# Optimization experiments

Measured on AMD Instinct MI355X. Metric: run time of the kernel, lower is better.

Reference implementation:

```python
import jax, jax.numpy as jnp
from jax import lax
import numpy as np

# Dims matching init_kwargs
V = 32000      # vocab
D = 768        # d_model
L = 4          # n_layers
N = 16         # state_size
K = 4          # conv kernel
I = 2 * D      # intermediate = expand * d_model = 1536
DT = (D + 15) // 16  # time_step_rank = 48
BATCH, SEQ = 4, 2048
EPS = 1e-5


def setup_inputs() -> dict:
    key = jax.random.key(0)
    ks = jax.random.split(key, 12)
    s = 0.02
    A_init = jnp.broadcast_to(jnp.arange(1, N + 1, dtype=jnp.float32), (L, I, N))
    return {
        "input_ids": jax.random.randint(ks[0], (BATCH, SEQ), 0, V, dtype=jnp.int32),
        "embed": jax.random.normal(ks[1], (V, D), jnp.float32) * s,        # tied lm_head
        "norm_w": jnp.ones((L, D), jnp.float32),
        "in_proj_w": jax.random.normal(ks[2], (L, 2 * I, D), jnp.float32) * s,
        "conv_w": jax.random.normal(ks[3], (L, I, K), jnp.float32) * s,
        "conv_b": jnp.zeros((L, I), jnp.float32),
        "x_proj_w": jax.random.normal(ks[4], (L, DT + 2 * N, I), jnp.float32) * s,
        "dt_proj_w": jax.random.normal(ks[5], (L, I, DT), jnp.float32) * s,
        "dt_proj_b": jax.random.normal(ks[6], (L, I), jnp.float32) * s,
        "A_log": jnp.log(A_init),
        "D_param": jnp.ones((L, I), jnp.float32),
        "out_proj_w": jax.random.normal(ks[7], (L, D, I), jnp.float32) * s,
        "norm_f_w": jnp.ones((D,), jnp.float32),
    }


def rmsnorm(x, w):
    return x * lax.rsqrt(jnp.mean(x * x, axis=-1, keepdims=True) + EPS) * w


def mamba_mixer(x, in_w, cw, cb, xp_w, dtp_w, dtp_b, a_log, d_par, out_w):
    # x: [B, S, D]
    proj = jnp.einsum('bsd,ed->bse', x, in_w)            # [B, S, 2I]
    u, gate = jnp.split(proj, 2, axis=-1)                # each [B, S, I]
    # causal depthwise conv1d (HF pads K-1 then truncates to S == left pad)
    uc = u.transpose(0, 2, 1)                            # [B, I, S]
    conv = lax.conv_general_dilated(
        uc, cw[:, None, :], window_strides=(1,), padding=[(K - 1, 0)],
        feature_group_count=I, dimension_numbers=('NCH', 'OIH', 'NCH'))
    ut = jax.nn.silu(conv + cb[None, :, None]).transpose(0, 2, 1)  # [B, S, I]
    # SSM parameters
    xdbl = jnp.einsum('bsi,ei->bse', ut, xp_w)           # [B, S, DT+2N]
    dt_r = xdbl[..., :DT]
    Bm = xdbl[..., DT:DT + N]                            # [B, S, N]
    Cm = xdbl[..., DT + N:]                              # [B, S, N]
    dt = jax.nn.softplus(jnp.einsum('bsr,ir->bsi', dt_r, dtp_w) + dtp_b)  # [B, S, I]
    A = -jnp.exp(a_log)                                  # [I, N]

    def step(h, ins):
        dt_t, B_t, C_t, u_t = ins                        # [B,I],[B,N],[B,N],[B,I]
        dA = jnp.exp(dt_t[..., None] * A)                # [B, I, N]
        h = dA * h + (dt_t[..., None] * B_t[:, None, :]) * u_t[..., None]
        y = jnp.einsum('bin,bn->bi', h, C_t)
        return h, y

    h0 = jnp.zeros((x.shape[0], I, N), x.dtype)
    xs = (dt.transpose(1, 0, 2), Bm.transpose(1, 0, 2),
          Cm.transpose(1, 0, 2), ut.transpose(1, 0, 2))
    _, ys = lax.scan(step, h0, xs)                       # [S, B, I]
    y = ys.transpose(1, 0, 2) + ut * d_par               # skip D term
    y = y * jax.nn.silu(gate)
    return jnp.einsum('bsi,di->bsd', y, out_w)           # [B, S, D]


def reference(input_ids, embed, norm_w, in_proj_w, conv_w, conv_b, x_proj_w,
              dt_proj_w, dt_proj_b, A_log, D_param, out_proj_w, norm_f_w):
    h = embed[input_ids]                                 # [B, S, D]
    for l in range(L):
        h = h + mamba_mixer(rmsnorm(h, norm_w[l]), in_proj_w[l], conv_w[l],
                            conv_b[l], x_proj_w[l], dt_proj_w[l], dt_proj_b[l],
                            A_log[l], D_param[l], out_proj_w[l])
    h = rmsnorm(h, norm_f_w)
    # module returns logits[:, -1]; compute only last-token logits (tied lm_head)
    return h[:, -1] @ embed.T                            # [B, V]
```

## Files before the change

### kernel.cpp

```cpp
#include <hip/hip_runtime.h>
#include <hip/hip_bf16.h>

#define Vv 32000
#define Dm 768
#define Lm 4
#define Nst 16
#define Kc 4
#define Im 1536
#define DTr 48
#define Bt 4
#define Sq 2048
#define TOK (Bt*Sq)
#define EPSf 1e-5f
#define NC 64
#define CL 32
#define QROWS (Bt*NC*16)
#define LOG2E 1.4426950408889634f
#define LN2f  0.6931471805599453f

using bf16 = __hip_bfloat16;
typedef __bf16 bf16x8 __attribute__((ext_vector_type(8)));
typedef float f32x4 __attribute__((ext_vector_type(4)));
typedef float f32x2 __attribute__((ext_vector_type(2)));

__device__ __forceinline__ float b2f(bf16 x){ return __bfloat162float(x); }
__device__ __forceinline__ bf16 f2b(float x){ return __float2bfloat16(x); }
__device__ __forceinline__ float us2f(ushort u){ unsigned x = (unsigned)u << 16; return __builtin_bit_cast(float, x); }

__device__ __forceinline__ float ex2(float x){
#if __has_builtin(__builtin_amdgcn_exp2f)
  return __builtin_amdgcn_exp2f(x);
#else
  float r; asm("v_exp_f32 %0, %1" : "=v"(r) : "v"(x)); return r;
#endif
}
__device__ __forceinline__ float vlog2(float x){
#if __has_builtin(__builtin_amdgcn_logf)
  return __builtin_amdgcn_logf(x);
#else
  float r; asm("v_log_f32 %0, %1" : "=v"(r) : "v"(x)); return r;
#endif
}
__device__ __forceinline__ float frcp(float x){
#if __has_builtin(__builtin_amdgcn_rcpf)
  return __builtin_amdgcn_rcpf(x);
#else
  float r; asm("v_rcp_f32 %0, %1" : "=v"(r) : "v"(x)); return r;
#endif
}

#define GLDS(gp, lp) __builtin_amdgcn_global_load_lds( \
    (const __attribute__((address_space(1))) void*)(gp), \
    (__attribute__((address_space(3))) void*)(lp), 16, 0, 0)

__global__ __launch_bounds__(256) void k_cvt(const float* __restrict__ src,
                                             bf16* __restrict__ dst, int n){
  int i = (blockIdx.x*256 + threadIdx.x)*4;
  if (i >= n) return;
  float4 v = *(const float4*)(src + i);
  bf16* o = dst + i;
  o[0]=f2b(v.x); o[1]=f2b(v.y); o[2]=f2b(v.z); o[3]=f2b(v.w);
}

__global__ __launch_bounds__(256) void k_cvt_xpw(const float* __restrict__ src,
                                                 bf16* __restrict__ dst){
  int idx = blockIdx.x*256 + threadIdx.x;
  int l = idx / (128*Im); int rem = idx - l*128*Im;
  int r = rem / Im;       int c = rem - r*Im;
  dst[idx] = (r < 80) ? f2b(src[((size_t)l*80 + r)*Im + c]) : f2b(0.f);
}

__global__ __launch_bounds__(256) void k_cvt_dtw(const float* __restrict__ src,
                                                 bf16* __restrict__ dst){
  int idx = blockIdx.x*256 + threadIdx.x;
  int l = idx / (Im*64); int rem = idx - l*Im*64;
  int r = rem / 64;      int c = rem - r*64;
  dst[idx] = (c < 48) ? f2b(src[((size_t)l*Im + r)*48 + c]) : f2b(0.f);
}

__global__ __launch_bounds__(256) void k_embed(const int* __restrict__ ids,
                                               const float* __restrict__ emb,
                                               float* __restrict__ h){
  int t = blockIdx.x;
  const float4* e = (const float4*)(emb + (size_t)ids[t]*Dm);
  float4* o = (float4*)(h + (size_t)t*Dm);
  if (threadIdx.x < Dm/4) o[threadIdx.x] = e[threadIdx.x];
}

__global__ __launch_bounds__(256) void k_rmsnorm(const float* __restrict__ h,
                                                 const float* __restrict__ w,
                                                 bf16* __restrict__ xb){
  int t = blockIdx.x;
  const float* x = h + (size_t)t*Dm;
  float v[3]; float ss = 0.f;
  #pragma unroll
  for (int j=0;j<3;j++){ v[j] = x[threadIdx.x + j*256]; ss += v[j]*v[j]; }
  #pragma unroll
  for (int off=32; off; off>>=1) ss += __shfl_xor(ss, off);
  __shared__ float sred[4];
  int wave = threadIdx.x>>6, lane = threadIdx.x&63;
  if (lane==0) sred[wave]=ss;
  __syncthreads();
  float tot = sred[0]+sred[1]+sred[2]+sred[3];
  float scale = rsqrtf(tot*(1.f/Dm) + EPSf);
  bf16* o = xb + (size_t)t*Dm;
  #pragma unroll
  for (int j=0;j<3;j++){ int d = threadIdx.x + j*256; o[d] = f2b(v[j]*scale*w[d]); }
}

__global__ __launch_bounds__(256) void k_rms_last(const float* __restrict__ h,
                                                  const float* __restrict__ w,
                                                  float* __restrict__ xf){
  int b = blockIdx.x;
  const float* x = h + ((size_t)b*Sq + (Sq-1))*Dm;
  float v[3]; float ss = 0.f;
  #pragma unroll
  for (int j=0;j<3;j++){ v[j] = x[threadIdx.x + j*256]; ss += v[j]*v[j]; }
  #pragma unroll
  for (int off=32; off; off>>=1) ss += __shfl_xor(ss, off);
  __shared__ float sred[4];
  int wave = threadIdx.x>>6, lane = threadIdx.x&63;
  if (lane==0) sred[wave]=ss;
  __syncthreads();
  float tot = sred[0]+sred[1]+sred[2]+sred[3];
  float scale = rsqrtf(tot*(1.f/Dm) + EPSf);
  float* o = xf + (size_t)b*Dm;
  #pragma unroll
  for (int j=0;j<3;j++){ int d = threadIdx.x + j*256; o[d] = v[j]*scale*w[d]; }
}

template<int MODE>
__global__ __launch_bounds__(256) void k_gemm(const bf16* __restrict__ A,
                                              const bf16* __restrict__ Bw,
                                              void* __restrict__ Cout,
                                              const float* __restrict__ bias,
                                              int M, int N, int K,
                                              int lda, int ldb, int ldc){
  __shared__ __align__(16) ushort Ash[128*32];
  __shared__ __align__(16) ushort Bsh[128*32];
  int tid = threadIdx.x;
  int bm = blockIdx.y, bn = blockIdx.x;
  int wave = tid >> 6, lane = tid & 63;
  int wrow = wave >> 1, wcol = wave & 1;
  int quad = lane >> 4, lq = lane & 15;

  f32x4 acc[4][4];
  #pragma unroll
  for (int a=0;a<4;a++)
    #pragma unroll
    for (int b=0;b<4;b++) acc[a][b] = (f32x4){0.f,0.f,0.f,0.f};

  const ushort* Ag = (const ushort*)A;
  const ushort* Bg = (const ushort*)Bw;

  for (int k0 = 0; k0 < K; k0 += 32) {
    __syncthreads();
    #pragma unroll
    for (int c = tid; c < 512; c += 256) {
      int row = c >> 2, col = (c & 3) * 8;
      GLDS(&Ag[(size_t)(bm*128 + row)*lda + k0 + col], &Ash[c*8]);
      GLDS(&Bg[(size_t)(bn*128 + row)*ldb + k0 + col], &Bsh[c*8]);
    }
    __syncthreads();
    bf16x8 af[4], bfr[4];
    #pragma unroll
    for (int a=0;a<4;a++){
      int m = wrow*64 + a*16 + lq;
      af[a] = __builtin_bit_cast(bf16x8, *(const uint4*)&Ash[m*32 + quad*8]);
    }
    #pragma unroll
    for (int b=0;b<4;b++){
      int n = wcol*64 + b*16 + lq;
      bfr[b] = __builtin_bit_cast(bf16x8, *(const uint4*)&Bsh[n*32 + quad*8]);
    }
    #pragma unroll
    for (int a=0;a<4;a++)
      #pragma unroll
      for (int b=0;b<4;b++)
        acc[a][b] = __builtin_amdgcn_mfma_f32_16x16x32_bf16(af[a], bfr[b], acc[a][b], 0, 0, 0);
  }
  #pragma unroll
  for (int a=0;a<4;a++)
    #pragma unroll
    for (int b=0;b<4;b++)
      #pragma unroll
      for (int r=0;r<4;r++){
        int row = bm*128 + wrow*64 + a*16 + quad*4 + r;
        int col = bn*128 + wcol*64 + b*16 + lq;
        size_t idx = (size_t)row*ldc + col;
        if (MODE == 0) ((bf16*)Cout)[idx] = f2b(acc[a][b][r]);
        else if (MODE == 1) ((float*)Cout)[idx] += acc[a][b][r];
        else {
          float v = acc[a][b][r] + bias[col];
          float sp;
          if (v > 20.f) sp = v;
          else { float e = ex2(v*LOG2E); sp = vlog2(1.f + e)*LN2f; }
          ((bf16*)Cout)[idx] = f2b(sp);
        }
      }
}

#define SA256(qm,k0s,bf_) { GLDS(Ag + sA[qm][0] + (k0s), lds + (bf_)*32768 + lA[qm][0]); \
                            GLDS(Ag + sA[qm][1] + (k0s), lds + (bf_)*32768 + lA[qm][1]); }
#define SB256(qn,k0s,bf_) { GLDS(Bg + sB[qn][0] + (k0s), lds + 65536 + (bf_)*32768 + lB[qn][0]); \
                            GLDS(Bg + sB[qn][1] + (k0s), lds + 65536 + (bf_)*32768 + lB[qn][1]); }
#define RD_A(qm_) do{ _Pragma("unroll") for(int m2=0;m2<4;m2++){ \
    int r = wm*128 + ((qm_)*4+m2)*16 + lq; \
    _Pragma("unroll") for(int kh=0;kh<2;kh++) \
      bA[m2][kh] = *(const uint4*)(Ab + (r<<7) + ((kh*64 + quad*16) ^ ((r&7)<<4))); } }while(0)
#define RD_B(qn_) do{ _Pragma("unroll") for(int n2=0;n2<2;n2++){ \
    int r = wn*64 + ((qn_)*2+n2)*16 + lq; \
    _Pragma("unroll") for(int kh=0;kh<2;kh++) \
      bB[qn_][n2][kh] = *(const uint4*)(Bb + (r<<7) + ((kh*64 + quad*16) ^ ((r&7)<<4))); } }while(0)
#define MMA256(qm_,qn_) do{ \
  __builtin_amdgcn_s_barrier(); \
  __builtin_amdgcn_sched_barrier(0); \
  __builtin_amdgcn_s_setprio(1); \
  _Pragma("unroll") for(int m2=0;m2<4;m2++) \
    _Pragma("unroll") for(int n2=0;n2<2;n2++) \
      _Pragma("unroll") for(int kh=0;kh<2;kh++) \
        acc[(qm_)*4+m2][(qn_)*2+n2] = __builtin_amdgcn_mfma_f32_16x16x32_bf16( \
          __builtin_bit_cast(bf16x8, bA[m2][kh]), __builtin_bit_cast(bf16x8, bB[qn_][n2][kh]), \
          acc[(qm_)*4+m2][(qn_)*2+n2], 0, 0, 0); \
  __builtin_amdgcn_s_setprio(0); \
  __builtin_amdgcn_s_barrier(); \
  __builtin_amdgcn_sched_barrier(0); \
}while(0)
#define VMW4 asm volatile("s_waitcnt vmcnt(4)":::"memory")

template<int MODE>
__global__ __launch_bounds__(512, 2) void k_gemm256(const bf16* __restrict__ A,
                                                    const bf16* __restrict__ Bw,
                                                    void* __restrict__ Cout,
                                                    int M, int N, int K,
                                                    int lda, int ldb, int ldc){
  __shared__ __align__(16) char lds[131072];
  int tid = threadIdx.x;
  int wave = tid >> 6, lane = tid & 63;
  int wm = wave >> 2, wn = wave & 3;
  int quad = lane >> 4, lq = lane & 15;
  int nx = gridDim.x;
  int nwg = nx * gridDim.y;
  int lin = blockIdx.y * nx + blockIdx.x;
  if ((nwg & 7) == 0){
    int cpx = nwg >> 3;
    lin = (lin & 7)*cpx + (lin >> 3);
  }
  int bm = lin / nx, bn = lin - bm*nx;
  const ushort* Ag = (const ushort*)A;
  const ushort* Bg = (const ushort*)Bw;

  size_t sA[2][2]; int lA[2][2];
  size_t sB[2][2]; int lB[2][2];
  #pragma unroll
  for (int qm=0; qm<2; qm++)
    #pragma unroll
    for (int d=0; d<2; d++){
      int r = d*128 + qm*64 + (tid>>3);
      int cb = ((tid&7)<<4) ^ ((r&7)<<4);
      sA[qm][d] = (size_t)(bm*256 + r)*lda + (cb>>1);
      lA[qm][d] = ((d*128 + qm*64)<<7) + tid*16;
    }
  #pragma unroll
  for (int qn=0; qn<2; qn++)
    #pragma unroll
    for (int d=0; d<2; d++){
      int g = 2*d + (wave>>2);
      int jj = tid & 255;
      int r = g*64 + qn*32 + (jj>>3);
      int cb = ((jj&7)<<4) ^ ((r&7)<<4);
      sB[qn][d] = (size_t)(bn*256 + r)*ldb + (cb>>1);
      lB[qn][d] = ((g*64 + qn*32)<<7) + jj*16;
    }

  f32x4 acc[8][4];
  #pragma unroll
  for (int a=0;a<8;a++)
    #pragma unroll
    for (int b=0;b<4;b++) acc[a][b] = (f32x4){0.f,0.f,0.f,0.f};

  SA256(0, 0, 0); SB256(0, 0, 0); SB256(1, 0, 0); SA256(1, 0, 0);
  VMW4;
  __builtin_amdgcn_s_barrier();
  __builtin_amdgcn_sched_barrier(0);

  uint4 bA[4][2], bB[2][2][2];
  int NT = K >> 6;
  for (int t = 0; t < NT-1; t++){
    int buf = t & 1, bufn = buf ^ 1;
    int k0n = (t+1) << 6;
    const char* Ab = lds + buf*32768;
    const char* Bb = lds + 65536 + buf*32768;
    RD_A(0); RD_B(0); SA256(0,k0n,bufn); VMW4; MMA256(0,0);
    RD_B(1);          SB256(0,k0n,bufn); VMW4; MMA256(0,1);
    RD_A(1);          SB256(1,k0n,bufn);       MMA256(1,0);
                      SA256(1,k0n,bufn); VMW4; MMA256(1,1);
  }
  {
    int buf = (NT-1) & 1;
    const char* Ab = lds + buf*32768;
    const char* Bb = lds + 65536 + buf*32768;
    RD_A(0); RD_B(0); asm volatile("s_waitcnt vmcnt(2)":::"memory"); MMA256(0,0);
    RD_B(1);          asm volatile("s_waitcnt vmcnt(0)":::"memory"); MMA256(0,1);
    RD_A(1);                                                          MMA256(1,0);
                                                                      MMA256(1,1);
  }

  #pragma unroll
  for (int mr=0; mr<8; mr++)
    #pragma unroll
    for (int nr=0; nr<4; nr++)
      #pragma unroll
      for (int rr=0; rr<4; rr++){
        int row = bm*256 + wm*128 + mr*16 + quad*4 + rr;
        int col = bn*256 + wn*64 + nr*16 + lq;
        size_t idx = (size_t)row*ldc + col;
        if (MODE == 0) ((bf16*)Cout)[idx] = f2b(acc[mr][nr][rr]);
        else ((float*)Cout)[idx] += acc[mr][nr][rr];
      }
}

__global__ __launch_bounds__(192) void k_conv8(const bf16* __restrict__ proj,
                                               const float* __restrict__ cw,
                                               const float* __restrict__ cb,
                                               bf16* __restrict__ ut){
  int t = blockIdx.x;
  int i = threadIdx.x*8;
  int s = t & (Sq-1);
  float acc[8];
  {
    float4 b0 = *(const float4*)(cb + i);
    float4 b1 = *(const float4*)(cb + i + 4);
    acc[0]=b0.x; acc[1]=b0.y; acc[2]=b0.z; acc[3]=b0.w;
    acc[4]=b1.x; acc[5]=b1.y; acc[6]=b1.z; acc[7]=b1.w;
  }
  float4 w[8];
  #pragma unroll
  for (int j=0;j<8;j++) w[j] = *(const float4*)(cw + (size_t)(i+j)*4);
  const ushort* pr = (const ushort*)proj + (size_t)t*(2*Im) + i;
  if (s >= 3){
    #pragma unroll
    for (int k=0;k<Kc;k++){
      uint4 v = *(const uint4*)(pr + (ptrdiff_t)(k-3)*(2*Im));
      const ushort* u = (const ushort*)&v;
      #pragma unroll
      for (int j=0;j<8;j++) acc[j] += us2f(u[j]) * (&w[j].x)[k];
    }
  } else {
    #pragma unroll
    for (int k=0;k<Kc;k++){
      if (s + k - 3 >= 0){
        uint4 v = *(const uint4*)(pr + (ptrdiff_t)(k-3)*(2*Im));
        const ushort* u = (const ushort*)&v;
        #pragma unroll
        for (int j=0;j<8;j++) acc[j] += us2f(u[j]) * (&w[j].x)[k];
      }
    }
  }
  ushort o[8];
  #pragma unroll
  for (int j=0;j<8;j++){
    float sig = frcp(1.f + ex2(-acc[j]*LOG2E));
    o[j] = __builtin_bit_cast(ushort, f2b(acc[j]*sig));
  }
  *(uint4*)((ushort*)ut + (size_t)t*Im + i) = *(const uint4*)o;
}


__global__ __launch_bounds__(256) void k_scan1(const bf16* __restrict__ dt,
                                               const bf16* __restrict__ ut,
                                               const bf16* __restrict__ xdbl,
                                               const float* __restrict__ alog,
                                               bf16* __restrict__ Qb,
                                               float* __restrict__ S){
  __shared__ float s_b[CL][16];
  int tid = threadIdx.x;
  int i = blockIdx.x*256 + tid;
  int b = blockIdx.y, c = blockIdx.z;
  size_t tok0 = (size_t)b*Sq + c*CL;
  {
    int row = tid >> 1, part = tid & 1;
    if (row < CL){
      uint4 v = *(const uint4*)((const ushort*)xdbl + (tok0+row)*128 + 48 + part*8);
      const ushort* u = (const ushort*)&v;
      #pragma unroll
      for (int j=0;j<8;j++) s_b[row][part*8+j] = us2f(u[j]);
    }
  }
  float kn[16];
  {
    const float4* ap = (const float4*)(alog + (size_t)i*16);
    #pragma unroll
    for (int q=0;q<4;q++){
      float4 a4 = ap[q];
      kn[q*4+0] = -__expf(a4.x)*LOG2E; kn[q*4+1] = -__expf(a4.y)*LOG2E;
      kn[q*4+2] = -__expf(a4.z)*LOG2E; kn[q*4+3] = -__expf(a4.w)*LOG2E;
    }
  }
  bool fastp = true;
  #pragma unroll
  for (int n=1;n<16;n++)
    fastp = fastp && (fabsf(kn[n] - (float)(n+1)*kn[0]) <= 1e-4f*fabsf(kn[n]));
  __syncthreads();
  float sum = 0.f;
  const ushort* dtp = (const ushort*)dt + tok0*Im + i;
  const ushort* utp = (const ushort*)ut + tok0*Im + i;
  ushort dA = dtp[0], uA = utp[0];
  ushort dB = dtp[Im], uB = utp[Im];
  int rq = (b*NC + c)*16;
  if (fastp){
    float k0 = kn[0];
    f32x2 h2[8];
    #pragma unroll
    for (int j=0;j<8;j++) h2[j] = (f32x2){0.f,0.f};
    for (int t = 0; t < CL; t++){
      float dtv = us2f(dA); float uv = us2f(uA);
      dA = dB; uA = uB;
      if (t+2 < CL){
        dB = dtp[(size_t)(t+2)*Im];
        uB = utp[(size_t)(t+2)*Im];
      }
      sum += dtv;
      float cdu = dtv*uv;
      f32x2 cdu2 = (f32x2){cdu, cdu};
      const f32x4* brow = (const f32x4*)&s_b[t][0];
      f32x4 B0=brow[0], B1=brow[1], B2=brow[2], B3=brow[3];
      f32x2 Bv2[8] = {
        __builtin_shufflevector(B0,B0,0,1), __builtin_shufflevector(B0,B0,2,3),
        __builtin_shufflevector(B1,B1,0,1), __builtin_shufflevector(B1,B1,2,3),
        __builtin_shufflevector(B2,B2,0,1), __builtin_shufflevector(B2,B2,2,3),
        __builtin_shufflevector(B3,B3,0,1), __builtin_shufflevector(B3,B3,2,3)};
      float p1 = ex2(k0*dtv);
      float p2 = p1*p1;
      f32x2 d2[8];
      d2[0] = (f32x2){p1,p2};
      f32x2 pp = (f32x2){p2,p2};
      d2[1] = d2[0]*pp;
      pp = (f32x2){d2[1][1], d2[1][1]};
      d2[2] = d2[0]*pp;
      d2[3] = d2[1]*pp;
      pp = (f32x2){d2[3][1], d2[3][1]};
      d2[4]=d2[0]*pp; d2[5]=d2[1]*pp; d2[6]=d2[2]*pp; d2[7]=d2[3]*pp;
      #pragma unroll
      for (int j=0;j<8;j++)
        h2[j] = d2[j]*h2[j] + cdu2*Bv2[j];
    }
    #pragma unroll
    for (int n=0;n<16;n++)
      Qb[(size_t)(rq+n)*2*Im + i] = f2b(h2[n>>1][n&1]);
  } else {
    float h[16];
    #pragma unroll
    for (int n=0;n<16;n++) h[n]=0.f;
    for (int t = 0; t < CL; t++){
      float dtv = us2f(dA); float uv = us2f(uA);
      dA = dB; uA = uB;
      if (t+2 < CL){
        dB = dtp[(size_t)(t+2)*Im];
        uB = utp[(size_t)(t+2)*Im];
      }
      sum += dtv;
      float cdu = dtv*uv;
      const f32x4* brow = (const f32x4*)&s_b[t][0];
      f32x4 B0=brow[0], B1=brow[1], B2=brow[2], B3=brow[3];
      float Bv[16] = {B0[0],B0[1],B0[2],B0[3],B1[0],B1[1],B1[2],B1[3],
                      B2[0],B2[1],B2[2],B2[3],B3[0],B3[1],B3[2],B3[3]};
      #pragma unroll
      for (int n=0;n<16;n++)
        h[n] = ex2(kn[n]*dtv)*h[n] + cdu*Bv[n];
    }
    #pragma unroll
    for (int n=0;n<16;n++)
      Qb[(size_t)(rq+n)*2*Im + i] = f2b(h[n]);
  }
  S[(size_t)(b*NC + c)*Im + i] = sum;
}

__global__ __launch_bounds__(256) void k_scan2(const bf16* __restrict__ Qb,
                                               const float* __restrict__ S,
                                               const float* __restrict__ alog,
                                               bf16* __restrict__ Hinb){
  int idx = blockIdx.x*256 + threadIdx.x;
  int i = idx % Im; int bn = idx / Im;
  int n = bn & 15, b = bn >> 4;
  float kn = -__expf(alog[(size_t)i*16 + n])*LOG2E;
  float h = 0.f;
  for (int c = 0; c < NC; c++){
    size_t r = (size_t)((b*NC + c)*16 + n);
    Hinb[(QROWS + r)*2*Im + i] = f2b(h);
    float P = ex2(kn * S[(size_t)(b*NC + c)*Im + i]);
    h = P*h + b2f(Qb[r*2*Im + i]);
  }
}

__global__ __launch_bounds__(256) void k_scan3(const bf16* __restrict__ dt,
                                               const bf16* __restrict__ ut,
                                               const bf16* __restrict__ xdbl,
                                               const bf16* __restrict__ proj,
                                               const float* __restrict__ alog,
                                               const float* __restrict__ dpar,
                                               const bf16* __restrict__ Hinb,
                                               bf16* __restrict__ y){
  __shared__ float s_bc[CL][32];
  int tid = threadIdx.x;
  int i = blockIdx.x*256 + tid;
  int b = blockIdx.y, c = blockIdx.z;
  size_t tok0 = (size_t)b*Sq + c*CL;
  {
    int row = tid >> 1, part = tid & 1;
    if (row < CL){
      const ushort* src = (const ushort*)xdbl + (tok0+row)*128 + 48 + part*16;
      uint4 v0 = *(const uint4*)src;
      uint4 v1 = *(const uint4*)(src + 8);
      const ushort* u0 = (const ushort*)&v0;
      const ushort* u1 = (const ushort*)&v1;
      #pragma unroll
      for (int j=0;j<8;j++){
        s_bc[row][part*16 + j]     = us2f(u0[j]);
        s_bc[row][part*16 + 8 + j] = us2f(u1[j]);
      }
    }
  }
  float kn[16];
  {
    const float4* ap = (const float4*)(alog + (size_t)i*16);
    #pragma unroll
    for (int q=0;q<4;q++){
      float4 a4 = ap[q];
      kn[q*4+0] = -__expf(a4.x)*LOG2E; kn[q*4+1] = -__expf(a4.y)*LOG2E;
      kn[q*4+2] = -__expf(a4.z)*LOG2E; kn[q*4+3] = -__expf(a4.w)*LOG2E;
    }
  }
  bool fastp = true;
  #pragma unroll
  for (int n=1;n<16;n++)
    fastp = fastp && (fabsf(kn[n] - (float)(n+1)*kn[0]) <= 1e-4f*fabsf(kn[n]));
  float Dp = dpar[i];
  int rq = QROWS + (b*NC + c)*16;
  __syncthreads();
  const ushort* dtp = (const ushort*)dt + tok0*Im + i;
  const ushort* utp = (const ushort*)ut + tok0*Im + i;
  const ushort* gp  = (const ushort*)proj + tok0*2*Im + Im + i;
  ushort dA = dtp[0], uA = utp[0], gA = gp[0];
  ushort dB = dtp[Im], uB = utp[Im], gB = gp[2*Im];
  if (fastp){
    float k0 = kn[0];
    f32x2 h2[8];
    #pragma unroll
    for (int j=0;j<8;j++)
      h2[j] = (f32x2){ b2f(Hinb[(size_t)(rq+2*j)*2*Im + i]),
                       b2f(Hinb[(size_t)(rq+2*j+1)*2*Im + i]) };
    for (int t = 0; t < CL; t++){
      float dtv = us2f(dA); float uv = us2f(uA); float g = us2f(gA);
      dA = dB; uA = uB; gA = gB;
      if (t+2 < CL){
        dB = dtp[(size_t)(t+2)*Im];
        uB = utp[(size_t)(t+2)*Im];
        gB = gp[(size_t)(t+2)*2*Im];
      }
      float cdu = dtv*uv;
      f32x2 cdu2 = (f32x2){cdu, cdu};
      const f32x4* brow = (const f32x4*)&s_bc[t][0];
      f32x4 B0=brow[0], B1=brow[1], B2=brow[2], B3=brow[3];
      f32x4 C0=brow[4], C1=brow[5], C2=brow[6], C3=brow[7];
      f32x2 Bv2[8] = {
        __builtin_shufflevector(B0,B0,0,1), __builtin_shufflevector(B0,B0,2,3),
        __builtin_shufflevector(B1,B1,0,1), __builtin_shufflevector(B1,B1,2,3),
        __builtin_shufflevector(B2,B2,0,1), __builtin_shufflevector(B2,B2,2,3),
        __builtin_shufflevector(B3,B3,0,1), __builtin_shufflevector(B3,B3,2,3)};
      f32x2 Cv2[8] = {
        __builtin_shufflevector(C0,C0,0,1), __builtin_shufflevector(C0,C0,2,3),
        __builtin_shufflevector(C1,C1,0,1), __builtin_shufflevector(C1,C1,2,3),
        __builtin_shufflevector(C2,C2,0,1), __builtin_shufflevector(C2,C2,2,3),
        __builtin_shufflevector(C3,C3,0,1), __builtin_shufflevector(C3,C3,2,3)};
      float p1 = ex2(k0*dtv);
      float p2 = p1*p1;
      f32x2 d2[8];
      d2[0] = (f32x2){p1,p2};
      f32x2 pp = (f32x2){p2,p2};
      d2[1] = d2[0]*pp;
      pp = (f32x2){d2[1][1], d2[1][1]};
      d2[2] = d2[0]*pp;
      d2[3] = d2[1]*pp;
      pp = (f32x2){d2[3][1], d2[3][1]};
      d2[4]=d2[0]*pp; d2[5]=d2[1]*pp; d2[6]=d2[2]*pp; d2[7]=d2[3]*pp;
      f32x2 yv2 = (f32x2){0.f, 0.f};
      #pragma unroll
      for (int j=0;j<8;j++){
        h2[j] = d2[j]*h2[j] + cdu2*Bv2[j];
        yv2 = yv2 + h2[j]*Cv2[j];
      }
      float yv = yv2[0] + yv2[1];
      float sig = frcp(1.f + ex2(-g*LOG2E));
      float outv = (yv + uv*Dp) * (g*sig);
      y[(tok0+t)*Im + i] = f2b(outv);
    }
  } else {
    float h[16];
    #pragma unroll
    for (int n=0;n<16;n++)
      h[n] = b2f(Hinb[(size_t)(rq+n)*2*Im + i]);
    for (int t = 0; t < CL; t++){
      float dtv = us2f(dA); float uv = us2f(uA); float g = us2f(gA);
      dA = dB; uA = uB; gA = gB;
      if (t+2 < CL){
        dB = dtp[(size_t)(t+2)*Im];
        uB = utp[(size_t)(t+2)*Im];
        gB = gp[(size_t)(t+2)*2*Im];
      }
      float cdu = dtv*uv;
      const f32x4* brow = (const f32x4*)&s_bc[t][0];
      f32x4 B0=brow[0], B1=brow[1], B2=brow[2], B3=brow[3];
      f32x4 C0=brow[4], C1=brow[5], C2=brow[6], C3=brow[7];
      float Bv[16] = {B0[0],B0[1],B0[2],B0[3],B1[0],B1[1],B1[2],B1[3],
                      B2[0],B2[1],B2[2],B2[3],B3[0],B3[1],B3[2],B3[3]};
      float Cv[16] = {C0[0],C0[1],C0[2],C0[3],C1[0],C1[1],C1[2],C1[3],
                      C2[0],C2[1],C2[2],C2[3],C3[0],C3[1],C3[2],C3[3]};
      float yv = 0.f;
      #pragma unroll
      for (int n=0;n<16;n++){
        h[n] = ex2(kn[n]*dtv)*h[n] + cdu*Bv[n];
        yv += h[n]*Cv[n];
      }
      float sig = frcp(1.f + ex2(-g*LOG2E));
      float outv = (yv + uv*Dp) * (g*sig);
      y[(tok0+t)*Im + i] = f2b(outv);
    }
  }
}

__global__ __launch_bounds__(256) void k_logits(const float* __restrict__ xf,
                                                const float* __restrict__ emb,
                                                float* __restrict__ out){
  __shared__ __align__(16) float xs[Bt*Dm];
  for (int j = threadIdx.x; j < Bt*Dm; j += 256) xs[j] = xf[j];
  __syncthreads();
  int wave = threadIdx.x>>6, lane = threadIdx.x&63;
  int v = blockIdx.x*4 + wave;
  const float4* e4 = (const float4*)(emb + (size_t)v*Dm);
  float a0=0.f,a1=0.f,a2=0.f,a3=0.f;
  for (int j = lane; j < Dm/4; j += 64){
    float4 ev = e4[j];
    float4 x0 = *(const float4*)&xs[j*4];
    float4 x1 = *(const float4*)&xs[Dm + j*4];
    float4 x2 = *(const float4*)&xs[2*Dm + j*4];
    float4 x3 = *(const float4*)&xs[3*Dm + j*4];
    a0 += ev.x*x0.x + ev.y*x0.y + ev.z*x0.z + ev.w*x0.w;
    a1 += ev.x*x1.x + ev.y*x1.y + ev.z*x1.z + ev.w*x1.w;
    a2 += ev.x*x2.x + ev.y*x2.y + ev.z*x2.z + ev.w*x2.w;
    a3 += ev.x*x3.x + ev.y*x3.y + ev.z*x3.z + ev.w*x3.w;
  }
  #pragma unroll
  for (int off=32; off; off>>=1){
    a0+=__shfl_xor(a0,off); a1+=__shfl_xor(a1,off);
    a2+=__shfl_xor(a2,off); a3+=__shfl_xor(a3,off);
  }
  if (lane==0){
    out[v]        = a0;
    out[Vv+v]     = a1;
    out[2*Vv+v]   = a2;
    out[3*Vv+v]   = a3;
  }
}

extern "C" void kernel_launch(void* const* d_in, const int* in_sizes, int n_in,
                              void* d_out, int out_size, void* d_ws, size_t ws_size,
                              hipStream_t stream){
  const int*   ids   = (const int*)d_in[0];
  const float* emb   = (const float*)d_in[1];
  const float* normw = (const float*)d_in[2];
  const float* inw   = (const float*)d_in[3];
  const float* cw    = (const float*)d_in[4];
  const float* cb    = (const float*)d_in[5];
  const float* xpw   = (const float*)d_in[6];
  const float* dtw   = (const float*)d_in[7];
  const float* dtb   = (const float*)d_in[8];
  const float* alog  = (const float*)d_in[9];
  const float* dpar  = (const float*)d_in[10];
  const float* outw  = (const float*)d_in[11];
  const float* normf = (const float*)d_in[12];
  float* out = (float*)d_out;

  char* p = (char*)d_ws;
  float* h    = (float*)p;  p += (size_t)TOK*Dm*4;
  bf16*  xb   = (bf16*)p;   p += (size_t)TOK*Dm*2;
  bf16*  proj = (bf16*)p;   p += (size_t)TOK*2*Im*2;
  bf16*  utb  = (bf16*)p;   p += (size_t)TOK*Im*2;
  bf16*  xdbl = (bf16*)p;   p += (size_t)TOK*128*2;
  bf16*  dtq  = (bf16*)p;   p += (size_t)TOK*Im*2;
  bf16*  yb   = (bf16*)p;   p += (size_t)TOK*Im*2;
  float* xf   = (float*)p;  p += (size_t)Bt*Dm*4;
  bf16*  inwb = (bf16*)p;   p += (size_t)Lm*2*Im*Dm*2;
  bf16*  outwb= (bf16*)p;   p += (size_t)Lm*Dm*Im*2;
  bf16*  xpwb = (bf16*)p;   p += (size_t)Lm*128*Im*2;
  bf16*  dtwb = (bf16*)p;   p += (size_t)Lm*Im*64*2;
  float* S = (float*)xb;

  { int n = Lm*2*Im*Dm; k_cvt<<<n/1024, 256, 0, stream>>>(inw, inwb, n); }
  { int n = Lm*Dm*Im;   k_cvt<<<n/1024, 256, 0, stream>>>(outw, outwb, n); }
  k_cvt_xpw<<<(Lm*128*Im)/256, 256, 0, stream>>>(xpw, xpwb);
  k_cvt_dtw<<<(Lm*Im*64)/256, 256, 0, stream>>>(dtw, dtwb);

  k_embed<<<TOK, 256, 0, stream>>>(ids, emb, h);

  for (int l = 0; l < Lm; l++){
    k_rmsnorm<<<TOK, 256, 0, stream>>>(h, normw + l*Dm, xb);
    k_gemm256<0><<<dim3((2*Im)/256, TOK/256), 512, 0, stream>>>(
        xb, inwb + (size_t)l*2*Im*Dm, proj, TOK, 2*Im, Dm, Dm, Dm, 2*Im);
    k_conv8<<<TOK, 192, 0, stream>>>(
        proj, cw + (size_t)l*Im*Kc, cb + (size_t)l*Im, utb);
    k_gemm<0><<<dim3(1, TOK/128), 256, 0, stream>>>(
        utb, xpwb + (size_t)l*128*Im, xdbl, nullptr, TOK, 128, Im, Im, Im, 128);
    k_gemm<3><<<dim3(Im/128, TOK/128), 256, 0, stream>>>(
        xdbl, dtwb + (size_t)l*Im*64, dtq, dtb + (size_t)l*Im, TOK, Im, 64, 128, 64, Im);
    k_scan1<<<dim3(Im/256, Bt, NC), 256, 0, stream>>>(
        dtq, utb, xdbl, alog + (size_t)l*Im*Nst, proj, S);
    k_scan2<<<(Bt*Nst*Im)/256, 256, 0, stream>>>(
        proj, S, alog + (size_t)l*Im*Nst, proj);
    k_scan3<<<dim3(Im/256, Bt, NC), 256, 0, stream>>>(
        dtq, utb, xdbl, proj, alog + (size_t)l*Im*Nst, dpar + (size_t)l*Im, proj, yb);
    k_gemm<1><<<dim3(Dm/128, TOK/128), 256, 0, stream>>>(
        yb, outwb + (size_t)l*Dm*Im, h, nullptr, TOK, Dm, Im, Im, Im, Dm);
  }

  k_rms_last<<<Bt, 256, 0, stream>>>(h, normf, xf);
  k_logits<<<Vv/4, 256, 0, stream>>>(xf, emb, out);
}
```

Baseline: 1.339 ms.

## Add 128x256-tile pipelined GEMM kernel for out_proj residual accumulation

Replaces the generic 128x128 GEMM used for the out_proj (with residual add into h) by a new 512-thread kernel using 128x256 tiles, direct global-to-LDS loads with XOR swizzle, double buffering, interleaved MFMA/load scheduling with barriers and priority hints, and a workgroup remap for L2 locality. The goal is higher MFMA utilization and better operand reuse on the M=8192, N=768, K=1536 GEMM. The grid shrinks to 3x64 workgroups of larger size, which may reduce occupancy balance across CUs.

```diff
diff --git a/kernel.cpp b/kernel.cpp
--- a/kernel.cpp
+++ b/kernel.cpp
@@ -320,6 +320,115 @@
       }
 }
 
+#define SAn(qm_,k0s,bf_) GLDS(Ag + snA[qm_] + (k0s), lds + (bf_)*16384 + lnA[qm_])
+#define SBn(k0s,bf_) { GLDS(Bg + snB[0] + (k0s), lds + 32768 + (bf_)*32768 + lnB[0]); \
+                       GLDS(Bg + snB[1] + (k0s), lds + 32768 + (bf_)*32768 + lnB[1]); \
+                       GLDS(Bg + snB[2] + (k0s), lds + 32768 + (bf_)*32768 + lnB[2]); \
+                       GLDS(Bg + snB[3] + (k0s), lds + 32768 + (bf_)*32768 + lnB[3]); }
+#define RDAn(h_) do{ _Pragma("unroll") for(int mf=0; mf<4; mf++){ \
+    int r = ((h_)*4+mf)*16 + lq; \
+    _Pragma("unroll") for(int kh=0;kh<2;kh++) \
+      bA[mf][kh] = *(const uint4*)(Ab + (r<<7) + ((kh*64 + quad*16) ^ ((r&7)<<4))); } }while(0)
+#define RDBn() do{ _Pragma("unroll") for(int n2=0;n2<2;n2++){ \
+    int r = wn*32 + n2*16 + lq; \
+    _Pragma("unroll") for(int kh=0;kh<2;kh++) \
+      bB[n2][kh] = *(const uint4*)(Bb + (r<<7) + ((kh*64 + quad*16) ^ ((r&7)<<4))); } }while(0)
+#define MMAn(h_,s_) do{ \
+  __builtin_amdgcn_s_barrier(); \
+  __builtin_amdgcn_sched_barrier(0); \
+  __builtin_amdgcn_s_setprio(1); \
+  _Pragma("unroll") for(int m2=0;m2<2;m2++) \
+    _Pragma("unroll") for(int n2=0;n2<2;n2++) \
+      _Pragma("unroll") for(int kh=0;kh<2;kh++) \
+        acc[(h_)*4+(s_)*2+m2][n2] = __builtin_amdgcn_mfma_f32_16x16x32_bf16( \
+          __builtin_bit_cast(bf16x8, bA[(s_)*2+m2][kh]), __builtin_bit_cast(bf16x8, bB[n2][kh]), \
+          acc[(h_)*4+(s_)*2+m2][n2], 0, 0, 0); \
+  __builtin_amdgcn_s_setprio(0); \
+  __builtin_amdgcn_s_barrier(); \
+  __builtin_amdgcn_sched_barrier(0); \
+}while(0)
+
+__global__ __launch_bounds__(512, 2) void k_gemm256n(const bf16* __restrict__ A,
+                                                     const bf16* __restrict__ Bw,
+                                                     float* __restrict__ Cout,
+                                                     int M, int N, int K,
+                                                     int lda, int ldb, int ldc){
+  __shared__ __align__(16) char lds[98304];
+  int tid = threadIdx.x;
+  int wave = tid >> 6, lane = tid & 63;
+  int wn = wave;
+  int quad = lane >> 4, lq = lane & 15;
+  int nx = gridDim.x;
+  int nwg = nx * gridDim.y;
+  int lin = blockIdx.y * nx + blockIdx.x;
+  if ((nwg & 7) == 0){
+    int cpx = nwg >> 3;
+    lin = (lin & 7)*cpx + (lin >> 3);
+  }
+  int bm = lin / nx, bn = lin - bm*nx;
+  const ushort* Ag = (const ushort*)A;
+  const ushort* Bg = (const ushort*)Bw;
+
+  size_t snA[2]; int lnA[2];
+  size_t snB[4]; int lnB[4];
+  #pragma unroll
+  for (int qm=0; qm<2; qm++){
+    int r = qm*64 + (tid>>3);
+    int cb = ((tid&7)<<4) ^ ((r&7)<<4);
+    snA[qm] = (size_t)(bm*128 + r)*lda + (cb>>1);
+    lnA[qm] = qm*8192 + tid*16;
+  }
+  #pragma unroll
+  for (int d=0; d<4; d++){
+    int r = d*64 + (tid>>3);
+    int cb = ((tid&7)<<4) ^ ((r&7)<<4);
+    snB[d] = (size_t)(bn*256 + r)*ldb + (cb>>1);
+    lnB[d] = d*8192 + tid*16;
+  }
+
+  f32x4 acc[8][2];
+  #pragma unroll
+  for (int a=0;a<8;a++){ acc[a][0] = (f32x4){0.f,0.f,0.f,0.f}; acc[a][1] = (f32x4){0.f,0.f,0.f,0.f}; }
+
+  SBn(0, 0); SAn(0, 0, 0); SAn(1, 0, 0);
+  asm volatile("s_waitcnt vmcnt(1)":::"memory");
+  __builtin_amdgcn_s_barrier();
+  __builtin_amdgcn_sched_barrier(0);
+
+  uint4 bA[4][2], bB[2][2];
+  int NT = K >> 6;
+  for (int t = 0; t < NT-1; t++){
+    int buf = t & 1, bufn = buf ^ 1;
+    int k0n = (t+1) << 6;
+    const char* Ab = lds + buf*16384;
+    const char* Bb = lds + 32768 + buf*32768;
+    RDAn(0); RDBn(); SBn(k0n,bufn); SAn(0,k0n,bufn);                        MMAn(0,0);
+    asm volatile("s_waitcnt vmcnt(5)":::"memory");                          MMAn(0,1);
+    RDAn(1); SAn(1,k0n,bufn);                                               MMAn(1,0);
+    asm volatile("s_waitcnt vmcnt(1)":::"memory");                          MMAn(1,1);
+  }
+  {
+    int buf = (NT-1) & 1;
+    const char* Ab = lds + buf*16384;
+    const char* Bb = lds + 32768 + buf*32768;
+    RDAn(0); RDBn();                                                        MMAn(0,0);
+    asm volatile("s_waitcnt vmcnt(0)":::"memory");                          MMAn(0,1);
+    RDAn(1);                                                                MMAn(1,0);
+                                                                            MMAn(1,1);
+  }
+
+  #pragma unroll
+  for (int mf=0; mf<8; mf++)
+    #pragma unroll
+    for (int n2=0; n2<2; n2++)
+      #pragma unroll
+      for (int rr=0; rr<4; rr++){
+        int row = bm*128 + mf*16 + quad*4 + rr;
+        int col = bn*256 + wn*32 + n2*16 + lq;
+        Cout[(size_t)row*ldc + col] += acc[mf][n2][rr];
+      }
+}
+
 __global__ __launch_bounds__(192) void k_conv8(const bf16* __restrict__ proj,
                                                const float* __restrict__ cw,
                                                const float* __restrict__ cb,
@@ -719,8 +828,8 @@
         proj, S, alog + (size_t)l*Im*Nst, proj);
     k_scan3<<<dim3(Im/256, Bt, NC), 256, 0, stream>>>(
         dtq, utb, xdbl, proj, alog + (size_t)l*Im*Nst, dpar + (size_t)l*Im, proj, yb);
-    k_gemm<1><<<dim3(Dm/128, TOK/128), 256, 0, stream>>>(
-        yb, outwb + (size_t)l*Dm*Im, h, nullptr, TOK, Dm, Im, Im, Im, Dm);
+    k_gemm256n<<<dim3(Dm/256, TOK/128), 512, 0, stream>>>(
+        yb, outwb + (size_t)l*Dm*Im, h, TOK, Dm, Im, Im, Im, Dm);
   }
 
   k_rms_last<<<Bt, 256, 0, stream>>>(h, normf, xf);
```

Result: faster. 1.300 ms (-2.9%).
